# Kernel tuning notes

Measured on AMD Instinct MI355X. Metric: run time of the kernel, lower is better.

## Reference

```python
import jax, jax.numpy as jnp
import numpy as np
from jax import lax

B = 8192
HS = 64        # hidden_size (output channels)
HS4 = HS + 4   # internal channel count (68)
K = 3          # conv kernel size


def setup_inputs() -> dict:
    key = jax.random.key(0)
    ks = jax.random.split(key, 16)
    def n(k, shape, s=1.0):
        return jax.random.normal(k, shape, dtype=jnp.float32) * s
    return {
        "x": n(ks[0], (B, HS, 6, 6)),
        "cell": n(ks[1], (B, 2)),
        "interspace_coord": n(ks[2], (B, 2, 6, 6)),
        "conv1_w": n(ks[3], (HS4, HS4, K, K), 0.05),
        "conv1_b": n(ks[4], (HS4,), 0.05),
        "conv3_w": n(ks[5], (HS4, HS4, K, K), 0.05),
        "conv3_b": n(ks[6], (HS4,), 0.05),
        "lin5_w": n(ks[7], (9 * HS, HS4 * 25), 0.02),
        "lin5_b": n(ks[8], (9 * HS,), 0.02),
        "lin4_w": n(ks[9], (9 * HS, HS4 * 16), 0.02),
        "lin4_b": n(ks[10], (9 * HS,), 0.02),
        "lin3_w": n(ks[11], (9 * HS, HS4 * 9), 0.02),
        "lin3_b": n(ks[12], (9 * HS,), 0.02),
        "final_w": n(ks[13], (HS, 9 * HS), 0.02),
        "final_b": n(ks[14], (HS,), 0.02),
    }


def _conv(z, w, b):
    # torch Conv2d with padding=k//2, stride 1 == SAME conv, NCHW/OIHW
    y = lax.conv_general_dilated(z, w, (1, 1), 'SAME',
                                 dimension_numbers=('NCHW', 'OIHW', 'NCHW'))
    return y + b[None, :, None, None]


def _corners(z, ws):
    # four corner windows, stacked on a new leading axis (corner-major)
    H, W = z.shape[-2:]
    return jnp.stack([z[..., :ws, :ws],
                      z[..., :ws, W - ws:],
                      z[..., H - ws:, :ws],
                      z[..., H - ws:, W - ws:]], axis=0)


def reference(x, cell, interspace_coord,
              conv1_w, conv1_b, conv3_w, conv3_b,
              lin5_w, lin5_b, lin4_w, lin4_b, lin3_w, lin3_b,
              final_w, final_b):
    Bn = x.shape[0]
    new_cell = jnp.broadcast_to(cell.reshape(Bn, -1)[:, :, None, None],
                                (Bn, 2, 6, 6))
    lins = {5: (lin5_w, lin5_b), 4: (lin4_w, lin4_b), 3: (lin3_w, lin3_b)}
    for ws in (5, 4, 3):
        z = jnp.concatenate([x, new_cell, interspace_coord], axis=1)  # [B,68,6,6]
        z = _corners(z, ws).reshape(-1, HS4, ws, ws)                  # [4B,68,ws,ws]
        z = jnp.sin(z) + jnp.cos(z)
        z = jax.nn.relu(_conv(z, conv1_w, conv1_b))
        z = jnp.sin(z) + jnp.cos(z)
        z = jax.nn.relu(_conv(z, conv3_w, conv3_b)).reshape(4, Bn, -1)
        Wl, bl = lins[ws]
        z = jax.nn.relu(z @ Wl.T + bl).reshape(4, Bn, HS, 3, 3)
        m = jnp.concatenate([z[0], z[1]], axis=-1)   # [B,64,3,6]
        n = jnp.concatenate([z[2], z[3]], axis=-1)
        x = jnp.concatenate([m, n], axis=-2)          # [B,64,6,6]
    ew = 3
    c = _corners(x, ew)                               # [4,B,64,3,3]
    c = c.reshape(4 * Bn, -1) @ final_w.T + final_b   # [4B,64]
    c = c.reshape(Bn, HS, 2, 2)                       # same flat-order reshape as torch
    xc = x[:, :, ew - 1:ew + 1, ew - 1:ew + 1]        # center 2x2
    return (xc * c).reshape(Bn, HS, -1)
```

## Files before the change

### kernel.cpp

```cpp
#include <hip/hip_runtime.h>
#include <hip/hip_bf16.h>
#include <cstdint>
#include <cstddef>

#define BN 8192
#define MTOT 32768

using bf16 = __hip_bfloat16;
typedef float f32x4 __attribute__((ext_vector_type(4)));
typedef short short8 __attribute__((ext_vector_type(8)));

__device__ __forceinline__ bf16 f2b(float v) { return __float2bfloat16(v); }
__device__ __forceinline__ float b2f(bf16 v) { return __bfloat162float(v); }
__device__ __forceinline__ float sincos_sum(float x) {
    return 1.41421356237f * __sinf(x + 0.78539816340f);
}

template<int WS> struct WsCfg;
template<> struct WsCfg<5> { static constexpr int KD = 1728, NP = 1792, KTRUE = 1700; };
template<> struct WsCfg<4> { static constexpr int KD = 1088, NP = 1152, KTRUE = 1088; };
template<> struct WsCfg<3> { static constexpr int KD = 640,  NP = 640,  KTRUE = 612;  };

__global__ __launch_bounds__(256)
void zprep_block(const float* __restrict__ xF, const float* __restrict__ cell,
                 const float* __restrict__ isc, bf16* __restrict__ Z,
                 int m0g, int CM)
{
    constexpr int KD = 1728, KTRUE = 1700;
    const int b = blockIdx.x, tid = threadIdx.x;
    __shared__ float s[68][37];

    for (int i = tid; i < 64 * 36; i += 256) {
        int ic = i / 36, off = i % 36;
        s[ic][off] = sincos_sum(xF[((size_t)b * 64 + ic) * 36 + off]);
    }
    if (tid < 2) {
        float t = sincos_sum(cell[b * 2 + tid]);
        #pragma unroll
        for (int off = 0; off < 36; off++) s[64 + tid][off] = t;
    }
    if (tid >= 64 && tid < 136) {
        int j = tid - 64;
        int ic = j / 36, off = j % 36;
        s[66 + ic][off] = sincos_sum(isc[((size_t)b * 2 + ic) * 36 + off]);
    }
    __syncthreads();

    for (int i = tid; i < 4 * KD; i += 256) {
        int q = i / KD, k = i % KD;
        int gm = q * BN + b;
        if (gm < m0g || gm >= m0g + CM) continue;
        float v = 0.f;
        if (k < KTRUE) {
            int pi = k / 68, ic = k % 68;
            int r = (q >> 1) + pi / 5;
            int c = (q & 1) + pi % 5;
            v = s[ic][r * 6 + c];
        }
        Z[(size_t)(gm - m0g) * KD + k] = f2b(v);
    }
}

template<int WSv>
__device__ __forceinline__ bf16 conv_elem(const float* __restrict__ src, int n, int k)
{
    constexpr int KTRUE = 68 * WSv * WSv;
    float v = 0.f;
    if (n < KTRUE && k < KTRUE) {
        int po = n / 68, oc = n % 68, ro = po / WSv, co = po % WSv;
        int pi = k / 68, ic = k % 68, ri = pi / WSv, ci = pi % WSv;
        int kr = ri - ro + 1, kc = ci - co + 1;
        if (kr >= 0 && kr < 3 && kc >= 0 && kc < 3)
            v = src[((oc * 68 + ic) * 3 + kr) * 3 + kc];
    }
    return f2b(v);
}
template<int WSv>
__device__ __forceinline__ bf16 lin_elem(const float* __restrict__ wl, int n, int k)
{
    constexpr int KTRUE = 68 * WSv * WSv;
    float v = 0.f;
    if (n < 576 && k < KTRUE) {
        int pi = k / 68, ic = k % 68;
        v = wl[(size_t)n * KTRUE + ic * (WSv * WSv) + pi];
    }
    return f2b(v);
}

__global__ void megabuild(const float* __restrict__ c1w, const float* __restrict__ c3w,
                          const float* __restrict__ l5w, const float* __restrict__ l4w,
                          const float* __restrict__ l3w, const float* __restrict__ fw,
                          const float* __restrict__ c1b, const float* __restrict__ c3b,
                          const float* __restrict__ bl5, const float* __restrict__ bl4,
                          const float* __restrict__ bl3, const float* __restrict__ bfin,
                          const float* __restrict__ cell, const float* __restrict__ isc,
                          bf16* __restrict__ w1d5, bf16* __restrict__ w3d5,
                          bf16* __restrict__ w1d4, bf16* __restrict__ w3d4,
                          bf16* __restrict__ w1d3, bf16* __restrict__ w3d3,
                          bf16* __restrict__ wl5p, bf16* __restrict__ wl4p,
                          bf16* __restrict__ wl3p, bf16* __restrict__ wfp,
                          float* __restrict__ bias,
                          bf16* __restrict__ Z4, bf16* __restrict__ Z3)
{
    constexpr unsigned S0 = 2u*1792*1728, S1 = 2u*1152*1088, S2 = 2u*640*640;
    constexpr unsigned S3 = 640u*1728, S4 = 640u*1088, S5 = 640u*640;
    constexpr unsigned S6 = 128u*576, S7 = 9216;
    constexpr unsigned S8 = 4u*8192*16*4, S9 = 4u*8192*9*4, S10 = 32768u*28;
    constexpr unsigned O1=S0, O2=O1+S1, O3=O2+S2, O4=O3+S3, O5=O4+S4, O6=O5+S5,
                       O7=O6+S6, O8=O7+S7, O9=O8+S8, O10=O9+S9, OT=O10+S10;
    unsigned e = blockIdx.x * 256u + threadIdx.x;
    if (e >= OT) return;
    if (e < O1) {
        constexpr unsigned per = 1792u*1728;
        unsigned i = (e < per) ? e : e - per;
        bf16* dst = (e < per) ? w1d5 : w3d5;
        const float* src = (e < per) ? c1w : c3w;
        dst[i] = conv_elem<5>(src, (int)(i / 1728u), (int)(i % 1728u));
    } else if (e < O2) {
        unsigned i0 = e - O1; constexpr unsigned per = 1152u*1088;
        unsigned i = (i0 < per) ? i0 : i0 - per;
        bf16* dst = (i0 < per) ? w1d4 : w3d4;
        const float* src = (i0 < per) ? c1w : c3w;
        dst[i] = conv_elem<4>(src, (int)(i / 1088u), (int)(i % 1088u));
    } else if (e < O3) {
        unsigned i0 = e - O2; constexpr unsigned per = 640u*640;
        unsigned i = (i0 < per) ? i0 : i0 - per;
        bf16* dst = (i0 < per) ? w1d3 : w3d3;
        const float* src = (i0 < per) ? c1w : c3w;
        dst[i] = conv_elem<3>(src, (int)(i / 640u), (int)(i % 640u));
    } else if (e < O4) {
        unsigned i = e - O3;
        wl5p[i] = lin_elem<5>(l5w, (int)(i / 1728u), (int)(i % 1728u));
    } else if (e < O5) {
        unsigned i = e - O4;
        wl4p[i] = lin_elem<4>(l4w, (int)(i / 1088u), (int)(i % 1088u));
    } else if (e < O6) {
        unsigned i = e - O5;
        wl3p[i] = lin_elem<3>(l3w, (int)(i / 640u), (int)(i % 640u));
    } else if (e < O7) {
        unsigned i = e - O6, n = i / 576u, k = i % 576u;
        wfp[i] = (n < 64u) ? f2b(fw[n * 576u + k]) : f2b(0.f);
    } else if (e < O8) {
        int i = (int)(e - O7);
        float v = 0.f;
        if (i < 1792)      { int n = i;        if (n < 1700) v = c1b[n % 68]; }
        else if (i < 3584) { int n = i - 1792; if (n < 1700) v = c3b[n % 68]; }
        else if (i < 4736) { int n = i - 3584; if (n < 1088) v = c1b[n % 68]; }
        else if (i < 5888) { int n = i - 4736; if (n < 1088) v = c3b[n % 68]; }
        else if (i < 6528) { int n = i - 5888; if (n < 612)  v = c1b[n % 68]; }
        else if (i < 7168) { int n = i - 6528; if (n < 612)  v = c3b[n % 68]; }
        else if (i < 7808) { int n = i - 7168; if (n < 576)  v = bl5[n]; }
        else if (i < 8448) { int n = i - 7808; if (n < 576)  v = bl4[n]; }
        else if (i < 9088) { int n = i - 8448; if (n < 576)  v = bl3[n]; }
        else               { int n = i - 9088; if (n < 64)   v = bfin[n]; }
        bias[i] = v;
    } else if (e < O9) {
        unsigned i = e - O8;
        int j = (int)(i & 3u); i >>= 2;
        int pi = (int)(i & 15u); i >>= 4;
        int b = (int)(i & 8191u); int q = (int)(i >> 13);
        float t;
        if (j < 2) t = cell[b * 2 + j];
        else {
            int r = (q >> 1) * 2 + pi / 4, c = (q & 1) * 2 + pi % 4;
            t = isc[((size_t)b * 2 + (j - 2)) * 36 + r * 6 + c];
        }
        Z4[((size_t)q * BN + b) * 1088 + pi * 68 + 64 + j] = f2b(sincos_sum(t));
    } else if (e < O10) {
        unsigned i = e - O9;
        int j = (int)(i & 3u); i >>= 2;
        int pi = (int)(i % 9u); i /= 9u;
        int b = (int)(i & 8191u); int q = (int)(i >> 13);
        float t;
        if (j < 2) t = cell[b * 2 + j];
        else {
            int r = (q >> 1) * 3 + pi / 3, c = (q & 1) * 3 + pi % 3;
            t = isc[((size_t)b * 2 + (j - 2)) * 36 + r * 6 + c];
        }
        Z3[((size_t)q * BN + b) * 640 + pi * 68 + 64 + j] = f2b(sincos_sum(t));
    } else {
        unsigned i = e - O10;
        int m = (int)(i / 28u), t = (int)(i % 28u);
        Z3[(size_t)m * 640 + 612 + t] = f2b(0.f);
    }
}

__device__ __forceinline__ void gload_lds16(const bf16* g, const bf16* lds_wave_base)
{
    unsigned off = (unsigned)(uintptr_t)lds_wave_base;
    off = __builtin_amdgcn_readfirstlane(off);
    __builtin_amdgcn_global_load_lds((const __attribute__((address_space(1))) unsigned int*)g,
                                     (__attribute__((address_space(3))) unsigned int*)off,
                                     16, 0, 0);
}

__device__ __forceinline__ int imin(int a, int b) { return a < b ? a : b; }
__device__ __forceinline__ int imax(int a, int b) { return a > b ? a : b; }

template<int EPI, int WS, int WN>
__global__ __launch_bounds__(256)
void gemm_bt(const bf16* __restrict__ A, const bf16* __restrict__ Bm, int KD,
             const float* __restrict__ bias, int ntiles,
             bf16* __restrict__ C, int ldc, int nlimit,
             int m0g, bf16* __restrict__ znext,
             const bf16* __restrict__ afin_xc, float* __restrict__ outp)
{
    __shared__ bf16 As[128 * 32];
    __shared__ bf16 Bs[128 * 32];
    const int tid = threadIdx.x;
    const int wave = tid >> 6, lane = tid & 63;
    const int l15 = lane & 15, lq = lane >> 4;
    const int wr = (wave >> 1) * 64, wc = (wave & 1) * 64;

    const int id = blockIdx.x;
    const int mt8 = (int)gridDim.x / (ntiles * 8);
    const int xcd = id & 7, local = id >> 3;
    const int m_idx = xcd * mt8 + local / ntiles;
    const int n_idx = local % ntiles;
    const int n0 = n_idx * 128, m0 = m_idx * 128;

    int nspans = 1, sbeg[4], send[4];
    sbeg[0] = 0; send[0] = KD;
    if (WS > 0) {
        int po_lo = imin(n0 / 68, WS * WS - 1);
        int po_hi = imin((n0 + 127) / 68, WS * WS - 1);
        int ro_lo = po_lo / WS, ro_hi = po_hi / WS;
        int r_lo = imax(ro_lo - 1, 0), r_hi = imin(ro_hi + 1, WS - 1);
        int ci_lo = 0, ci_hi = WS - 1;
        if (ro_lo == ro_hi) {
            ci_lo = imax(po_lo % WS - 1, 0);
            ci_hi = imin(po_hi % WS + 1, WS - 1);
        }
        if (ci_lo == 0 && ci_hi == WS - 1) {
            sbeg[0] = (r_lo * WS * 68) & ~31;
            send[0] = imin(KD, ((r_hi + 1) * WS * 68 + 31) & ~31);
        } else {
            nspans = 0;
            for (int ri = r_lo; ri <= r_hi; ri++) {
                sbeg[nspans] = ((ri * WS + ci_lo) * 68) & ~31;
                send[nspans] = imin(KD, (((ri * WS + ci_hi + 1) * 68) + 31) & ~31);
                nspans++;
            }
        }
    }

    float bj[4];
    #pragma unroll
    for (int j = 0; j < 4; j++) bj[j] = bias[n0 + wc + j * 16 + l15];

    const bf16* Ab = A + (size_t)m0 * KD;
    const bf16* Bb = Bm + (size_t)n0 * KD;
    const int srow = tid >> 2, scol = (tid & 3) * 8;
    const bf16* aG0 = Ab + (size_t)srow * KD + scol;
    const bf16* aG1 = Ab + (size_t)(srow + 64) * KD + scol;
    const bf16* bG0 = Bb + (size_t)srow * KD + scol;
    const bf16* bG1 = Bb + (size_t)(srow + 64) * KD + scol;
    const bf16* lA0 = &As[wave * 512];
    const bf16* lA1 = &As[2048 + wave * 512];
    const bf16* lB0 = &Bs[wave * 512];
    const bf16* lB1 = &Bs[2048 + wave * 512];

    f32x4 acc[4][4];
    #pragma unroll
    for (int i = 0; i < 4; i++)
        #pragma unroll
        for (int j = 0; j < 4; j++) { f32x4 z = {0.f, 0.f, 0.f, 0.f}; acc[i][j] = z; }

    for (int s = 0; s < nspans; s++) {
        for (int k0 = sbeg[s]; k0 < send[s]; k0 += 32) {
            gload_lds16(aG0 + k0, lA0);
            gload_lds16(aG1 + k0, lA1);
            gload_lds16(bG0 + k0, lB0);
            gload_lds16(bG1 + k0, lB1);
            __syncthreads();
            short8 af[4], bg[4];
            #pragma unroll
            for (int i = 0; i < 4; i++) af[i] = *(const short8*)&As[(wr + i * 16 + l15) * 32 + lq * 8];
            #pragma unroll
            for (int j = 0; j < 4; j++) bg[j] = *(const short8*)&Bs[(wc + j * 16 + l15) * 32 + lq * 8];
            #pragma unroll
            for (int i = 0; i < 4; i++)
                #pragma unroll
                for (int j = 0; j < 4; j++)
                    acc[i][j] = __builtin_amdgcn_mfma_f32_16x16x32_bf16(af[i], bg[j], acc[i][j], 0, 0, 0);
            __syncthreads();
        }
    }

    #pragma unroll
    for (int i = 0; i < 4; i++) {
        #pragma unroll
        for (int j = 0; j < 4; j++) {
            int n = n0 + wc + j * 16 + l15;
            #pragma unroll
            for (int r = 0; r < 4; r++) {
                int m = m0 + wr + i * 16 + lq * 4 + r;
                float v = acc[i][j][r];
                if (EPI == 0) {
                    if (n < nlimit) {
                        v += bj[j]; v = fmaxf(v, 0.f); v = sincos_sum(v);
                        C[(size_t)m * ldc + n] = f2b(v);
                    }
                } else if (EPI == 1) {
                    if (n < nlimit) {
                        v += bj[j]; v = fmaxf(v, 0.f);
                        C[(size_t)m * ldc + n] = f2b(v);
                    }
                } else if (EPI == 2) {
                    if (n < 576) {
                        v += bj[j]; v = fmaxf(v, 0.f);
                        bf16 t = f2b(sincos_sum(v));
                        int gm = m0g + m;
                        int q = gm >> 13, b = gm & (BN - 1);
                        int ch = n / 9, p = n % 9;
                        int R = p / 3 + (q >> 1) * 3, Cc = p % 3 + (q & 1) * 3;
                        constexpr int OFF = 6 - WN;
                        constexpr int KDN = (WN == 4) ? 1088 : 640;
                        #pragma unroll
                        for (int qr = 0; qr < 2; qr++) {
                            int rr = R - OFF * qr;
                            if (rr < 0 || rr >= WN) continue;
                            #pragma unroll
                            for (int qc = 0; qc < 2; qc++) {
                                int cc = Cc - OFF * qc;
                                if (cc < 0 || cc >= WN) continue;
                                int pi = rr * WN + cc;
                                znext[((size_t)((qr * 2 + qc) * BN + b)) * KDN + pi * 68 + ch] = t;
                            }
                        }
                    }
                } else {
                    if (n < 64) {
                        v += bj[j];
                        int gm = m0g + m;
                        int f = gm * 64 + n;
                        int b2 = f >> 8, rem = f & 255;
                        int ch2 = rem >> 2, ii = (rem >> 1) & 1, jj = rem & 1;
                        int qq = ii * 2 + jj;
                        const int offt[4] = {8, 6, 2, 0};
                        float xc = b2f(afin_xc[((size_t)qq * BN + b2) * 576 + ch2 * 9 + offt[qq]]);
                        outp[f] = v * xc;
                    }
                }
            }
        }
    }
}

extern "C" void kernel_launch(void* const* d_in, const int* in_sizes, int n_in,
                              void* d_out, int out_size, void* d_ws, size_t ws_size,
                              hipStream_t stream)
{
    const float* x    = (const float*)d_in[0];
    const float* cell = (const float*)d_in[1];
    const float* isc  = (const float*)d_in[2];
    const float* c1w  = (const float*)d_in[3];
    const float* c1b  = (const float*)d_in[4];
    const float* c3w  = (const float*)d_in[5];
    const float* c3b  = (const float*)d_in[6];
    const float* l5w  = (const float*)d_in[7];
    const float* l5b  = (const float*)d_in[8];
    const float* l4w  = (const float*)d_in[9];
    const float* l4b  = (const float*)d_in[10];
    const float* l3w  = (const float*)d_in[11];
    const float* l3b  = (const float*)d_in[12];
    const float* fw   = (const float*)d_in[13];
    const float* fb   = (const float*)d_in[14];

    char* base = (char*)d_ws;
    size_t cur = 0;
    auto take = [&](size_t bytes) -> char* {
        char* r = base + cur; cur += (bytes + 255) & ~(size_t)255; return r;
    };

    const size_t Z4B = (size_t)MTOT * 1088 * 2;
    const size_t Z3B = (size_t)MTOT * 640 * 2;
    const size_t AFB = (size_t)MTOT * 576 * 2;
    size_t wbytes = 2 * (1792ull * 1728 + 1152ull * 1088 + 640ull * 640) * 2
                  + (640ull * 1728 + 640ull * 1088 + 640ull * 640) * 2
                  + 128ull * 576 * 2 + 9216ull * 4 + 64 * 256;
    auto need = [&](int nc) -> size_t {
        return Z4B + Z3B + AFB + wbytes + 2 * ((size_t)(MTOT / nc) * 1728 * 2);
    };
    int nchunk = (ws_size >= need(1)) ? 1 : (ws_size >= need(2)) ? 2
               : (ws_size >= need(4)) ? 4 : (ws_size >= need(8)) ? 8 : 16;

    bf16* Z4   = (bf16*)take(Z4B);
    bf16* Z3   = (bf16*)take(Z3B);
    bf16* afinb = (bf16*)take(AFB);
    bf16* w1d5 = (bf16*)take(1792ull * 1728 * 2);
    bf16* w3d5 = (bf16*)take(1792ull * 1728 * 2);
    bf16* w1d4 = (bf16*)take(1152ull * 1088 * 2);
    bf16* w3d4 = (bf16*)take(1152ull * 1088 * 2);
    bf16* w1d3 = (bf16*)take(640ull * 640 * 2);
    bf16* w3d3 = (bf16*)take(640ull * 640 * 2);
    bf16* wl5p = (bf16*)take(640ull * 1728 * 2);
    bf16* wl4p = (bf16*)take(640ull * 1088 * 2);
    bf16* wl3p = (bf16*)take(640ull * 640 * 2);
    bf16* wfp  = (bf16*)take(128ull * 576 * 2);
    float* biasb = (float*)take(9216ull * 4);
    int CM = MTOT / nchunk;
    int mt = CM / 128;
    bf16* Za = (bf16*)take((size_t)CM * 1728 * 2);
    bf16* Zb = (bf16*)take((size_t)CM * 1728 * 2);

    {
        constexpr unsigned OT = 2u*1792*1728 + 2u*1152*1088 + 2u*640*640
                              + 640u*1728 + 640u*1088 + 640u*640 + 128u*576 + 9216
                              + 4u*8192*16*4 + 4u*8192*9*4 + 32768u*28;
        megabuild<<<(OT + 255) / 256, 256, 0, stream>>>(
            c1w, c3w, l5w, l4w, l3w, fw, c1b, c3b, l5b, l4b, l3b, fb, cell, isc,
            w1d5, w3d5, w1d4, w3d4, w1d3, w3d3, wl5p, wl4p, wl3p, wfp, biasb, Z4, Z3);
    }

    for (int c = 0; c < nchunk; c++) {
        int m0g = c * CM;
        zprep_block<<<BN, 256, 0, stream>>>(x, cell, isc, Za, m0g, CM);
        gemm_bt<0, 5, 0><<<14 * mt, 256, 0, stream>>>(Za, w1d5, 1728, biasb + 0, 14,
                                                      Zb, 1728, 1728, 0, nullptr, nullptr, nullptr);
        gemm_bt<1, 5, 0><<<14 * mt, 256, 0, stream>>>(Zb, w3d5, 1728, biasb + 1792, 14,
                                                      Za, 1728, 1728, 0, nullptr, nullptr, nullptr);
        gemm_bt<2, 0, 4><<<5 * mt, 256, 0, stream>>>(Za, wl5p, 1728, biasb + 7168, 5,
                                                     nullptr, 0, 0, m0g, Z4, nullptr, nullptr);
    }
    for (int c = 0; c < nchunk; c++) {
        int m0g = c * CM;
        gemm_bt<0, 4, 0><<<9 * mt, 256, 0, stream>>>(Z4 + (size_t)m0g * 1088, w1d4, 1088,
                                                     biasb + 3584, 9, Zb, 1088, 1088,
                                                     0, nullptr, nullptr, nullptr);
        gemm_bt<1, 4, 0><<<9 * mt, 256, 0, stream>>>(Zb, w3d4, 1088, biasb + 4736, 9,
                                                     Za, 1088, 1088, 0, nullptr, nullptr, nullptr);
        gemm_bt<2, 0, 3><<<5 * mt, 256, 0, stream>>>(Za, wl4p, 1088, biasb + 7808, 5,
                                                     nullptr, 0, 0, m0g, Z3, nullptr, nullptr);
    }
    for (int c = 0; c < nchunk; c++) {
        int m0g = c * CM;
        gemm_bt<0, 3, 0><<<5 * mt, 256, 0, stream>>>(Z3 + (size_t)m0g * 640, w1d3, 640,
                                                     biasb + 5888, 5, Zb, 640, 640,
                                                     0, nullptr, nullptr, nullptr);
        gemm_bt<1, 3, 0><<<5 * mt, 256, 0, stream>>>(Zb, w3d3, 640, biasb + 6528, 5,
                                                     Za, 640, 640, 0, nullptr, nullptr, nullptr);
        gemm_bt<1, 0, 0><<<5 * mt, 256, 0, stream>>>(Za, wl3p, 640, biasb + 8448, 5,
                                                     afinb + (size_t)m0g * 576, 576, 576,
                                                     0, nullptr, nullptr, nullptr);
    }
    for (int c = 0; c < nchunk; c++) {
        int m0g = c * CM;
        gemm_bt<3, 0, 0><<<mt, 256, 0, stream>>>(afinb + (size_t)m0g * 576, wfp, 576,
                                                 biasb + 9088, 1, nullptr, 0, 0, m0g,
                                                 nullptr, afinb, (float*)d_out);
    }
}
```

Before: 1.336 ms.

## Add 512x128-tile triple-buffered GEMM kernel with 8 waves for conv/linear stages

Adds a new GEMM kernel that uses 512 threads and a 512x128 output tile per block, so each B tile loaded from memory is reused across four times as many rows. K-tiles are triple-buffered with direct global-to-LDS loads, and the MFMA work is split into two halves with barriers and partial vmcnt waits so loads overlap compute. The host picks this path whenever the workspace fits chunking of 8 or fewer and keeps the old kernel as a fallback. In exchange it uses much larger LDS (~120KB per block) and 32 accumulators per lane, which lowers occupancy, and the larger M tile leaves fewer blocks per launch.

```diff
diff --git a/kernel.cpp b/kernel.cpp
--- a/kernel.cpp
+++ b/kernel.cpp
@@ -16,10 +16,6 @@
     return 1.41421356237f * __sinf(x + 0.78539816340f);
 }
 
-template<int WS> struct WsCfg;
-template<> struct WsCfg<5> { static constexpr int KD = 1728, NP = 1792, KTRUE = 1700; };
-template<> struct WsCfg<4> { static constexpr int KD = 1088, NP = 1152, KTRUE = 1088; };
-template<> struct WsCfg<3> { static constexpr int KD = 640,  NP = 640,  KTRUE = 612;  };
 
 __global__ __launch_bounds__(256)
 void zprep_block(const float* __restrict__ xF, const float* __restrict__ cell,
@@ -198,6 +194,204 @@
 __device__ __forceinline__ int imax(int a, int b) { return a > b ? a : b; }
 
 template<int EPI, int WS, int WN>
+__global__ __launch_bounds__(512, 2)
+void gemm8(const bf16* __restrict__ A, const bf16* __restrict__ Bm, int KD,
+           const float* __restrict__ bias, int ntiles,
+           bf16* __restrict__ C, int ldc, int nlimit,
+           int m0g, bf16* __restrict__ znext)
+{
+    __shared__ bf16 As[3][16384];
+    __shared__ bf16 Bs[3][4096];
+    const int tid = threadIdx.x;
+    const int wave = tid >> 6, lane = tid & 63;
+    const int l15 = lane & 15, lq = lane >> 4;
+    const int wr = wave * 64;
+
+    const int id = blockIdx.x;
+    const int mt8 = (int)gridDim.x / (ntiles * 8);
+    const int xcd = id & 7, local = id >> 3;
+    const int m_idx = xcd * mt8 + local / ntiles;
+    const int n_idx = local % ntiles;
+    const int n0 = n_idx * 128, m0 = m_idx * 512;
+
+    int s0b = 0, s0e = KD, s1b = 0, s1e = 0, s2b = 0, s2e = 0;
+    if (WS > 0) {
+        int po_lo = imin(n0 / 68, WS * WS - 1);
+        int po_hi = imin((n0 + 127) / 68, WS * WS - 1);
+        int ro_lo = po_lo / WS, ro_hi = po_hi / WS;
+        int r_lo = imax(ro_lo - 1, 0), r_hi = imin(ro_hi + 1, WS - 1);
+        int ci_lo = 0, ci_hi = WS - 1;
+        if (ro_lo == ro_hi) {
+            ci_lo = imax(po_lo % WS - 1, 0);
+            ci_hi = imin(po_hi % WS + 1, WS - 1);
+        }
+        if (ci_lo == 0 && ci_hi == WS - 1) {
+            s0b = (r_lo * WS * 68) & ~31;
+            s0e = imin(KD, ((r_hi + 1) * WS * 68 + 31) & ~31);
+        } else {
+            s0b = ((r_lo * WS + ci_lo) * 68) & ~31;
+            s0e = imin(KD, (((r_lo * WS + ci_hi + 1) * 68) + 31) & ~31);
+            if (r_hi > r_lo) {
+                s1b = (((r_lo + 1) * WS + ci_lo) * 68) & ~31;
+                s1e = imin(KD, ((((r_lo + 1) * WS + ci_hi + 1) * 68) + 31) & ~31);
+            }
+            if (r_hi > r_lo + 1) {
+                s2b = (((r_lo + 2) * WS + ci_lo) * 68) & ~31;
+                s2e = imin(KD, ((((r_lo + 2) * WS + ci_hi + 1) * 68) + 31) & ~31);
+            }
+        }
+    }
+    const int c0 = (s0e - s0b) >> 5;
+    const int c1 = c0 + ((s1e - s1b) >> 5);
+    const int nt = c1 + ((s2e - s2b) >> 5);
+    auto k0_of = [&](int t2) -> int {
+        int k = s0b + (t2 << 5);
+        if (t2 >= c0) k = s1b + ((t2 - c0) << 5);
+        if (t2 >= c1) k = s2b + ((t2 - c1) << 5);
+        return k;
+    };
+
+    const int srow = tid >> 2;
+    const int sc8 = (tid & 3) ^ (srow & 3);
+    const bf16* aSrc = A + (size_t)(m0 + srow) * KD + sc8 * 8;
+    const bf16* bSrc = Bm + (size_t)(n0 + srow) * KD + sc8 * 8;
+    const int sOff = srow * 32 + (tid & 3) * 8;
+
+    auto stageA01 = [&](int k0, int buf) {
+        gload_lds16(aSrc + k0, &As[buf][sOff]);
+        gload_lds16(aSrc + k0 + (size_t)128 * KD, &As[buf][sOff + 4096]);
+    };
+    auto stageA23 = [&](int k0, int buf) {
+        gload_lds16(aSrc + k0 + (size_t)256 * KD, &As[buf][sOff + 8192]);
+        gload_lds16(aSrc + k0 + (size_t)384 * KD, &As[buf][sOff + 12288]);
+    };
+    auto stageB = [&](int k0, int buf) {
+        gload_lds16(bSrc + k0, &Bs[buf][sOff]);
+    };
+
+    const int lrA = wr + l15;
+    const int offA0 = lrA * 32 + ((lq ^ (lrA & 3)) * 8);
+    const int offB0 = l15 * 32 + ((lq ^ (l15 & 3)) * 8);
+
+    f32x4 acc[4][8];
+    #pragma unroll
+    for (int i = 0; i < 4; i++)
+        #pragma unroll
+        for (int j = 0; j < 8; j++) { f32x4 z = {0.f, 0.f, 0.f, 0.f}; acc[i][j] = z; }
+
+    {
+        const int k0a = k0_of(0);
+        stageA01(k0a, 0); stageA23(k0a, 0); stageB(k0a, 0);
+        if (nt > 1) {
+            const int k0b = k0_of(1);
+            stageA01(k0b, 1); stageA23(k0b, 1); stageB(k0b, 1);
+        }
+        __syncthreads();
+    }
+
+    for (int t = 0; t < nt; ++t) {
+        const int cur = t % 3;
+        const int nx = (t + 2) % 3;
+        const bool pf = (t + 2) < nt;
+        int k2 = 0;
+        if (pf) k2 = k0_of(t + 2);
+
+        const bf16* Ac = &As[cur][0];
+        const bf16* Bc = &Bs[cur][0];
+
+        short8 af[4], bg[4];
+        #pragma unroll
+        for (int i = 0; i < 4; i++) af[i] = *(const short8*)&Ac[offA0 + i * 512];
+        #pragma unroll
+        for (int j = 0; j < 4; j++) bg[j] = *(const short8*)&Bc[offB0 + j * 512];
+        if (pf) stageA01(k2, nx);
+        __builtin_amdgcn_s_barrier();
+        asm volatile("s_waitcnt lgkmcnt(0)" ::: "memory");
+        __builtin_amdgcn_sched_barrier(0);
+        __builtin_amdgcn_s_setprio(1);
+        #pragma unroll
+        for (int i = 0; i < 4; i++)
+            #pragma unroll
+            for (int j = 0; j < 4; j++)
+                acc[i][j] = __builtin_amdgcn_mfma_f32_16x16x32_bf16(af[i], bg[j], acc[i][j], 0, 0, 0);
+        __builtin_amdgcn_s_setprio(0);
+        __builtin_amdgcn_s_barrier();
+
+        short8 bh[4];
+        #pragma unroll
+        for (int j = 0; j < 4; j++) bh[j] = *(const short8*)&Bc[offB0 + (j + 4) * 512];
+        if (pf) {
+            stageA23(k2, nx); stageB(k2, nx);
+            asm volatile("s_waitcnt vmcnt(5)" ::: "memory");
+        } else {
+            asm volatile("s_waitcnt vmcnt(0)" ::: "memory");
+        }
+        __builtin_amdgcn_s_barrier();
+        asm volatile("s_waitcnt lgkmcnt(0)" ::: "memory");
+        __builtin_amdgcn_sched_barrier(0);
+        __builtin_amdgcn_s_setprio(1);
+        #pragma unroll
+        for (int i = 0; i < 4; i++)
+            #pragma unroll
+            for (int j = 0; j < 4; j++)
+                acc[i][j + 4] = __builtin_amdgcn_mfma_f32_16x16x32_bf16(af[i], bh[j], acc[i][j + 4], 0, 0, 0);
+        __builtin_amdgcn_s_setprio(0);
+        __builtin_amdgcn_s_barrier();
+    }
+
+    float bj[8];
+    #pragma unroll
+    for (int j = 0; j < 8; j++) bj[j] = bias[n0 + j * 16 + l15];
+
+    #pragma unroll
+    for (int i = 0; i < 4; i++) {
+        #pragma unroll
+        for (int j = 0; j < 8; j++) {
+            int n = n0 + j * 16 + l15;
+            #pragma unroll
+            for (int r = 0; r < 4; r++) {
+                int m = m0 + wr + i * 16 + lq * 4 + r;
+                float v = acc[i][j][r];
+                if (EPI == 0) {
+                    if (n < nlimit) {
+                        v += bj[j]; v = fmaxf(v, 0.f); v = sincos_sum(v);
+                        C[(size_t)m * ldc + n] = f2b(v);
+                    }
+                } else if (EPI == 1) {
+                    if (n < nlimit) {
+                        v += bj[j]; v = fmaxf(v, 0.f);
+                        C[(size_t)m * ldc + n] = f2b(v);
+                    }
+                } else {
+                    if (n < 576) {
+                        v += bj[j]; v = fmaxf(v, 0.f);
+                        bf16 tv = f2b(sincos_sum(v));
+                        int gm = m0g + m;
+                        int q = gm >> 13, b = gm & (BN - 1);
+                        int ch = n / 9, p = n % 9;
+                        int R = p / 3 + (q >> 1) * 3, Cc = p % 3 + (q & 1) * 3;
+                        constexpr int OFF = 6 - WN;
+                        constexpr int KDN = (WN == 4) ? 1088 : 640;
+                        #pragma unroll
+                        for (int qr = 0; qr < 2; qr++) {
+                            int rr = R - OFF * qr;
+                            if (rr < 0 || rr >= WN) continue;
+                            #pragma unroll
+                            for (int qc = 0; qc < 2; qc++) {
+                                int cc = Cc - OFF * qc;
+                                if (cc < 0 || cc >= WN) continue;
+                                int pi = rr * WN + cc;
+                                znext[((size_t)((qr * 2 + qc) * BN + b)) * KDN + pi * 68 + ch] = tv;
+                            }
+                        }
+                    }
+                }
+            }
+        }
+    }
+}
+
+template<int EPI, int WS, int WN>
 __global__ __launch_bounds__(256)
 void gemm_bt(const bf16* __restrict__ A, const bf16* __restrict__ Bm, int KD,
              const float* __restrict__ bias, int ntiles,
@@ -382,8 +576,10 @@
     auto need = [&](int nc) -> size_t {
         return Z4B + Z3B + AFB + wbytes + 2 * ((size_t)(MTOT / nc) * 1728 * 2);
     };
-    int nchunk = (ws_size >= need(1)) ? 1 : (ws_size >= need(2)) ? 2
-               : (ws_size >= need(4)) ? 4 : (ws_size >= need(8)) ? 8 : 16;
+    const bool use8 = (ws_size >= need(8));
+    int nchunk = use8 ? ((ws_size >= need(1)) ? 1 : (ws_size >= need(2)) ? 2
+                       : (ws_size >= need(4)) ? 4 : 8)
+                      : 16;
 
     bf16* Z4   = (bf16*)take(Z4B);
     bf16* Z3   = (bf16*)take(Z3B);
@@ -401,6 +597,7 @@
     float* biasb = (float*)take(9216ull * 4);
     int CM = MTOT / nchunk;
     int mt = CM / 128;
+    int mt5 = CM / 512;
     bf16* Za = (bf16*)take((size_t)CM * 1728 * 2);
     bf16* Zb = (bf16*)take((size_t)CM * 1728 * 2);
 
@@ -413,36 +610,70 @@
             w1d5, w3d5, w1d4, w3d4, w1d3, w3d3, wl5p, wl4p, wl3p, wfp, biasb, Z4, Z3);
     }
 
-    for (int c = 0; c < nchunk; c++) {
-        int m0g = c * CM;
-        zprep_block<<<BN, 256, 0, stream>>>(x, cell, isc, Za, m0g, CM);
-        gemm_bt<0, 5, 0><<<14 * mt, 256, 0, stream>>>(Za, w1d5, 1728, biasb + 0, 14,
-                                                      Zb, 1728, 1728, 0, nullptr, nullptr, nullptr);
-        gemm_bt<1, 5, 0><<<14 * mt, 256, 0, stream>>>(Zb, w3d5, 1728, biasb + 1792, 14,
-                                                      Za, 1728, 1728, 0, nullptr, nullptr, nullptr);
-        gemm_bt<2, 0, 4><<<5 * mt, 256, 0, stream>>>(Za, wl5p, 1728, biasb + 7168, 5,
-                                                     nullptr, 0, 0, m0g, Z4, nullptr, nullptr);
-    }
-    for (int c = 0; c < nchunk; c++) {
-        int m0g = c * CM;
-        gemm_bt<0, 4, 0><<<9 * mt, 256, 0, stream>>>(Z4 + (size_t)m0g * 1088, w1d4, 1088,
-                                                     biasb + 3584, 9, Zb, 1088, 1088,
-                                                     0, nullptr, nullptr, nullptr);
-        gemm_bt<1, 4, 0><<<9 * mt, 256, 0, stream>>>(Zb, w3d4, 1088, biasb + 4736, 9,
-                                                     Za, 1088, 1088, 0, nullptr, nullptr, nullptr);
-        gemm_bt<2, 0, 3><<<5 * mt, 256, 0, stream>>>(Za, wl4p, 1088, biasb + 7808, 5,
-                                                     nullptr, 0, 0, m0g, Z3, nullptr, nullptr);
-    }
-    for (int c = 0; c < nchunk; c++) {
-        int m0g = c * CM;
-        gemm_bt<0, 3, 0><<<5 * mt, 256, 0, stream>>>(Z3 + (size_t)m0g * 640, w1d3, 640,
-                                                     biasb + 5888, 5, Zb, 640, 640,
-                                                     0, nullptr, nullptr, nullptr);
-        gemm_bt<1, 3, 0><<<5 * mt, 256, 0, stream>>>(Zb, w3d3, 640, biasb + 6528, 5,
-                                                     Za, 640, 640, 0, nullptr, nullptr, nullptr);
-        gemm_bt<1, 0, 0><<<5 * mt, 256, 0, stream>>>(Za, wl3p, 640, biasb + 8448, 5,
-                                                     afinb + (size_t)m0g * 576, 576, 576,
-                                                     0, nullptr, nullptr, nullptr);
+    if (use8) {
+        for (int c = 0; c < nchunk; c++) {
+            int m0g = c * CM;
+            zprep_block<<<BN, 256, 0, stream>>>(x, cell, isc, Za, m0g, CM);
+            gemm8<0, 5, 0><<<14 * mt5, 512, 0, stream>>>(Za, w1d5, 1728, biasb + 0, 14,
+                                                         Zb, 1728, 1728, 0, nullptr);
+            gemm8<1, 5, 0><<<14 * mt5, 512, 0, stream>>>(Zb, w3d5, 1728, biasb + 1792, 14,
+                                                         Za, 1728, 1728, 0, nullptr);
+            gemm8<2, 0, 4><<<5 * mt5, 512, 0, stream>>>(Za, wl5p, 1728, biasb + 7168, 5,
+                                                        nullptr, 0, 0, m0g, Z4);
+        }
+        for (int c = 0; c < nchunk; c++) {
+            int m0g = c * CM;
+            gemm8<0, 4, 0><<<9 * mt5, 512, 0, stream>>>(Z4 + (size_t)m0g * 1088, w1d4, 1088,
+                                                        biasb + 3584, 9, Zb, 1088, 1088,
+                                                        0, nullptr);
+            gemm8<1, 4, 0><<<9 * mt5, 512, 0, stream>>>(Zb, w3d4, 1088, biasb + 4736, 9,
+                                                        Za, 1088, 1088, 0, nullptr);
+            gemm8<2, 0, 3><<<5 * mt5, 512, 0, stream>>>(Za, wl4p, 1088, biasb + 7808, 5,
+                                                        nullptr, 0, 0, m0g, Z3);
+        }
+        for (int c = 0; c < nchunk; c++) {
+            int m0g = c * CM;
+            gemm8<0, 3, 0><<<5 * mt5, 512, 0, stream>>>(Z3 + (size_t)m0g * 640, w1d3, 640,
+                                                        biasb + 5888, 5, Zb, 640, 640,
+                                                        0, nullptr);
+            gemm8<1, 3, 0><<<5 * mt5, 512, 0, stream>>>(Zb, w3d3, 640, biasb + 6528, 5,
+                                                        Za, 640, 640, 0, nullptr);
+            gemm8<1, 0, 0><<<5 * mt5, 512, 0, stream>>>(Za, wl3p, 640, biasb + 8448, 5,
+                                                        afinb + (size_t)m0g * 576, 576, 576,
+                                                        0, nullptr);
+        }
+    } else {
+        for (int c = 0; c < nchunk; c++) {
+            int m0g = c * CM;
+            zprep_block<<<BN, 256, 0, stream>>>(x, cell, isc, Za, m0g, CM);
+            gemm_bt<0, 5, 0><<<14 * mt, 256, 0, stream>>>(Za, w1d5, 1728, biasb + 0, 14,
+                                                          Zb, 1728, 1728, 0, nullptr, nullptr, nullptr);
+            gemm_bt<1, 5, 0><<<14 * mt, 256, 0, stream>>>(Zb, w3d5, 1728, biasb + 1792, 14,
+                                                          Za, 1728, 1728, 0, nullptr, nullptr, nullptr);
+            gemm_bt<2, 0, 4><<<5 * mt, 256, 0, stream>>>(Za, wl5p, 1728, biasb + 7168, 5,
+                                                         nullptr, 0, 0, m0g, Z4, nullptr, nullptr);
+        }
+        for (int c = 0; c < nchunk; c++) {
+            int m0g = c * CM;
+            gemm_bt<0, 4, 0><<<9 * mt, 256, 0, stream>>>(Z4 + (size_t)m0g * 1088, w1d4, 1088,
+                                                         biasb + 3584, 9, Zb, 1088, 1088,
+                                                         0, nullptr, nullptr, nullptr);
+            gemm_bt<1, 4, 0><<<9 * mt, 256, 0, stream>>>(Zb, w3d4, 1088, biasb + 4736, 9,
+                                                         Za, 1088, 1088, 0, nullptr, nullptr, nullptr);
+            gemm_bt<2, 0, 3><<<5 * mt, 256, 0, stream>>>(Za, wl4p, 1088, biasb + 7808, 5,
+                                                         nullptr, 0, 0, m0g, Z3, nullptr, nullptr);
+        }
+        for (int c = 0; c < nchunk; c++) {
+            int m0g = c * CM;
+            gemm_bt<0, 3, 0><<<5 * mt, 256, 0, stream>>>(Z3 + (size_t)m0g * 640, w1d3, 640,
+                                                         biasb + 5888, 5, Zb, 640, 640,
+                                                         0, nullptr, nullptr, nullptr);
+            gemm_bt<1, 3, 0><<<5 * mt, 256, 0, stream>>>(Zb, w3d3, 640, biasb + 6528, 5,
+                                                         Za, 640, 640, 0, nullptr, nullptr, nullptr);
+            gemm_bt<1, 0, 0><<<5 * mt, 256, 0, stream>>>(Za, wl3p, 640, biasb + 8448, 5,
+                                                         afinb + (size_t)m0g * 576, 576, 576,
+                                                         0, nullptr, nullptr, nullptr);
+        }
     }
     for (int c = 0; c < nchunk; c++) {
         int m0g = c * CM;
```

Measured after the change: 1.426 ms. 1.07x slower.
